# Kernel optimization log

Measured on AMD Instinct MI355X. Metric: run time of the kernel, lower is better.

Reference implementation:

```python
import jax, jax.numpy as jnp
import numpy as np

HEADS = 8
DIM_HEAD = 64
QLEVEL = 127.0  # symmetric int8: clamp to [-128, 127]


def fake_quant(x):
    """Symmetric per-tensor int8 fake quantization with straight-through estimator."""
    delta = jnp.max(jnp.abs(x)) / QLEVEL
    xq = jnp.clip(jnp.round(x / delta), -128.0, 127.0) * delta
    return x + jax.lax.stop_gradient(xq - x)


def setup_inputs() -> dict:
    key = jax.random.key(0)
    ks = jax.random.split(key, 7)
    b, n, m, d, dc = 2, 4096, 1024, 512, 768
    return {
        "x": jax.random.normal(ks[0], (b, n, d), jnp.float32),
        "context": jax.random.normal(ks[1], (b, m, dc), jnp.float32),
        "Wq": jax.random.normal(ks[2], (d, d), jnp.float32) * 0.02,
        "Wk": jax.random.normal(ks[3], (dc, d), jnp.float32) * 0.02,
        "Wv": jax.random.normal(ks[4], (dc, d), jnp.float32) * 0.02,
        "Wo": jax.random.normal(ks[5], (d, d), jnp.float32) * 0.02,
        "bo": jnp.zeros((d,), jnp.float32),
    }


def reference(x, context, Wq, Wk, Wv, Wo, bo):
    b, n, _ = x.shape
    h, dh = HEADS, DIM_HEAD
    scale = dh ** -0.5

    q = x @ Wq            # [b, n, h*dh]
    k = context @ Wk      # [b, m, h*dh]
    v = context @ Wv      # [b, m, h*dh]

    def split(t):  # b n (h d) -> b h n d
        return t.reshape(t.shape[0], t.shape[1], h, dh).transpose(0, 2, 1, 3)

    q, k, v = split(q), split(k), split(v)

    # fake-quantize q and k before the score matmul (use_aq=True path)
    q = fake_quant(q)
    k = fake_quant(k)
    sim = jnp.einsum('bhid,bhjd->bhij', q, k) * scale  # [b, h, n, m]
    attn = jax.nn.softmax(sim, axis=-1)

    # fake-quantize attention weights and v before the AV matmul
    out = jnp.einsum('bhij,bhjd->bhid', fake_quant(attn), fake_quant(v))
    out = out.transpose(0, 2, 1, 3).reshape(b, n, h * dh)  # b h n d -> b n (h d)
    return out @ Wo + bo  # to_out[0]; to_out[-1] is Dropout (identity in eval)
```

## Files before the change

kernel.cpp:

```cpp
#include <hip/hip_runtime.h>
#include <stdint.h>

typedef float  v4f  __attribute__((ext_vector_type(4)));
typedef int    v4i  __attribute__((ext_vector_type(4)));
typedef __bf16 v8bf __attribute__((ext_vector_type(8)));
typedef __bf16 v4bf __attribute__((ext_vector_type(4)));

#define BATCH  2
#define NQ     4096
#define MK     1024
#define DMODEL 512
#define DCTX   768
#define NH     8
#define DH     64

__global__ __launch_bounds__(256) void k_wtrans(
    const float* __restrict__ Wq, const float* __restrict__ Wk,
    const float* __restrict__ Wv, const float* __restrict__ Wo,
    __bf16* __restrict__ Wq_t, __bf16* __restrict__ Wk_t,
    __bf16* __restrict__ Wv_t, __bf16* __restrict__ Wo_t,
    unsigned* __restrict__ scal) {
  if (blockIdx.x == 0 && blockIdx.y == 0 && blockIdx.z == 0 && threadIdx.x < 4)
    scal[threadIdx.x] = 0u;
  const float* src; __bf16* dst; int K;
  switch (blockIdx.z) {
    case 0:  src = Wq; dst = Wq_t; K = DMODEL; break;
    case 1:  src = Wk; dst = Wk_t; K = DCTX;   break;
    case 2:  src = Wv; dst = Wv_t; K = DCTX;   break;
    default: src = Wo; dst = Wo_t; K = DMODEL; break;
  }
  int k0 = blockIdx.y * 32;
  if (k0 >= K) return;
  int n0 = blockIdx.x * 32;
  __shared__ __bf16 tile[32][33];
  int c = threadIdx.x & 31, r0 = threadIdx.x >> 5;
  for (int i = 0; i < 4; ++i) {
    int r = r0 + i * 8;
    tile[c][r] = (__bf16)src[(size_t)(k0 + r) * DMODEL + n0 + c];
  }
  __syncthreads();
  for (int i = 0; i < 4; ++i) {
    int r = r0 + i * 8;
    dst[(size_t)(n0 + r) * K + k0 + c] = tile[r][c];
  }
}

template<bool BIAS, bool AMAX>
__global__ __launch_bounds__(256, 4) void k_gemm64(
    const float* __restrict__ A, const __bf16* __restrict__ Bt,
    float* __restrict__ C, int M, int N, int K,
    const float* __restrict__ bias,
    unsigned* __restrict__ amaxLo, unsigned* __restrict__ amaxHi) {
  __shared__ __bf16 As[64 * 76];
  __shared__ __bf16 Bs[64 * 76];
  __shared__ float redmax[4];
  const int tid = threadIdx.x;
  const int lane = tid & 63, wave = tid >> 6;
  const int l15 = lane & 15, g = lane >> 4;
  const int row0 = blockIdx.x * 64, col0 = blockIdx.y * 64;
  const int wrow = (wave >> 1) * 32, wcol = (wave & 1) * 32;

  v4f acc[2][2] = {};

  for (int k0 = 0; k0 < K; k0 += 64) {
#pragma unroll
    for (int i = 0; i < 4; ++i) {
      int f = tid + 256 * i;
      int r = f >> 4, c4 = (f & 15) << 2;
      float4 av = *(const float4*)(A + (size_t)(row0 + r) * K + k0 + c4);
      v4bf ap = { (__bf16)av.x, (__bf16)av.y, (__bf16)av.z, (__bf16)av.w };
      *(v4bf*)(&As[r * 76 + c4]) = ap;
    }
#pragma unroll
    for (int i = 0; i < 2; ++i) {
      int f = tid + 256 * i;
      int r = f >> 3, c8 = (f & 7) << 3;
      *(v8bf*)(&Bs[r * 76 + c8]) =
          *(const v8bf*)(Bt + (size_t)(col0 + r) * K + k0 + c8);
    }
    __syncthreads();
#pragma unroll
    for (int c = 0; c < 2; ++c) {
      v8bf af0 = *(const v8bf*)(&As[(wrow + l15) * 76 + c * 32 + g * 8]);
      v8bf af1 = *(const v8bf*)(&As[(wrow + 16 + l15) * 76 + c * 32 + g * 8]);
      v8bf bf0 = *(const v8bf*)(&Bs[(wcol + l15) * 76 + c * 32 + g * 8]);
      v8bf bf1 = *(const v8bf*)(&Bs[(wcol + 16 + l15) * 76 + c * 32 + g * 8]);
      acc[0][0] = __builtin_amdgcn_mfma_f32_16x16x32_bf16(af0, bf0, acc[0][0], 0, 0, 0);
      acc[0][1] = __builtin_amdgcn_mfma_f32_16x16x32_bf16(af0, bf1, acc[0][1], 0, 0, 0);
      acc[1][0] = __builtin_amdgcn_mfma_f32_16x16x32_bf16(af1, bf0, acc[1][0], 0, 0, 0);
      acc[1][1] = __builtin_amdgcn_mfma_f32_16x16x32_bf16(af1, bf1, acc[1][1], 0, 0, 0);
    }
    __syncthreads();
  }

  float lmax = 0.0f;
#pragma unroll
  for (int j = 0; j < 2; ++j) {
    int col = col0 + wcol + j * 16 + l15;
    float bv = BIAS ? bias[col] : 0.0f;
#pragma unroll
    for (int i = 0; i < 2; ++i) {
#pragma unroll
      for (int r = 0; r < 4; ++r) {
        int row = row0 + wrow + i * 16 + g * 4 + r;
        float cv = acc[i][j][r] + bv;
        C[(size_t)row * N + col] = cv;
        if (AMAX) lmax = fmaxf(lmax, fabsf(cv));
      }
    }
  }
  if (AMAX) {
    for (int off = 32; off > 0; off >>= 1)
      lmax = fmaxf(lmax, __shfl_xor(lmax, off, 64));
    if (lane == 0) redmax[wave] = lmax;
    __syncthreads();
    if (tid == 0) {
      float bm = fmaxf(fmaxf(redmax[0], redmax[1]), fmaxf(redmax[2], redmax[3]));
      atomicMax(col0 < 512 ? amaxLo : amaxHi, __float_as_uint(bm));
    }
  }
}

__global__ __launch_bounds__(256) void k_quant_all(
    const float* __restrict__ qf, const float* __restrict__ kvf,
    int8_t* __restrict__ q8, int8_t* __restrict__ k8, int8_t* __restrict__ v8t,
    const unsigned* __restrict__ scal) {
  __shared__ int8_t tile[64][80];
  int bx = blockIdx.x;
  if (bx < 5120) {
    float4 v; int8_t* dst; float s;
    if (bx < 4096) {
      int idx = bx * 256 + threadIdx.x;
      v = ((const float4*)qf)[idx];
      dst = q8 + (size_t)idx * 4;
      s = 127.0f / __uint_as_float(scal[0]);
    } else {
      int j = (bx - 4096) * 256 + threadIdx.x;
      int r = j >> 7;
      int c4 = (j & 127) << 2;
      v = *(const float4*)(kvf + (size_t)r * 1024 + c4);
      dst = k8 + (size_t)j * 4;
      s = 127.0f / __uint_as_float(scal[1]);
    }
    int a0 = __float2int_rn(v.x * s), a1 = __float2int_rn(v.y * s);
    int a2 = __float2int_rn(v.z * s), a3 = __float2int_rn(v.w * s);
    a0 = max(-128, min(127, a0)); a1 = max(-128, min(127, a1));
    a2 = max(-128, min(127, a2)); a3 = max(-128, min(127, a3));
    unsigned p = (unsigned)(a0 & 255) | ((unsigned)(a1 & 255) << 8) |
                 ((unsigned)(a2 & 255) << 16) | ((unsigned)(a3 & 255) << 24);
    *(unsigned*)dst = p;
    return;
  }
  int id = bx - 5120;
  int bh = id >> 4, b = bh >> 3, h = bh & 7;
  int j0 = (id & 15) * 64;
  const float s = 127.0f / __uint_as_float(scal[2]);
  int t = threadIdx.x;
  int j = t >> 2, dh0 = (t & 3) << 4;
  const float* src = kvf + (size_t)(b * MK + j0 + j) * 1024 + 512 + h * DH + dh0;
#pragma unroll
  for (int i = 0; i < 16; i += 4) {
    float4 v = *(const float4*)(src + i);
    int a0 = __float2int_rn(v.x * s), a1 = __float2int_rn(v.y * s);
    int a2 = __float2int_rn(v.z * s), a3 = __float2int_rn(v.w * s);
    tile[dh0 + i + 0][j] = (int8_t)max(-128, min(127, a0));
    tile[dh0 + i + 1][j] = (int8_t)max(-128, min(127, a1));
    tile[dh0 + i + 2][j] = (int8_t)max(-128, min(127, a2));
    tile[dh0 + i + 3][j] = (int8_t)max(-128, min(127, a3));
  }
  __syncthreads();
  int dh = t >> 2, jb = (t & 3) << 4;
  v4i val = *(const v4i*)(&tile[dh][jb]);
  *(v4i*)(v8t + (size_t)(bh * DH + dh) * MK + j0 + jb) = val;
}

__global__ __launch_bounds__(256, 4) void k_pass1(
    const int8_t* __restrict__ q8, const int8_t* __restrict__ k8,
    float* __restrict__ invz, unsigned* __restrict__ scal) {
  __shared__ float zbuf[4][64];
  __shared__ int   mbuf[4][64];
  int bh = blockIdx.y, b = bh >> 3, h = bh & 7;
  int wave = threadIdx.x >> 6, lane = threadIdx.x & 63;
  int l15 = lane & 15, g = lane >> 4;
  int row0 = blockIdx.x * 64;
  const float aq = __uint_as_float(scal[0]), ak = __uint_as_float(scal[1]);
  const float alpha2 = (aq * ak) * (0.125f / (127.0f * 127.0f)) * 1.44269504f;
  const v4i z4 = {0, 0, 0, 0};
  v4i qfrag[4];
#pragma unroll
  for (int rg = 0; rg < 4; ++rg)
    qfrag[rg] = *(const v4i*)(q8 + (size_t)(b * NQ + row0 + rg * 16 + l15) * DMODEL + h * DH + g * 16);
  const int8_t* kbase = k8 + (size_t)b * MK * DMODEL + h * DH + g * 16 +
                        (size_t)wave * 256 * DMODEL;
  v4i kf[16];
#pragma unroll
  for (int i = 0; i < 16; ++i)
    kf[i] = *(const v4i*)(kbase + (size_t)(i * 16 + l15) * DMODEL);

  float z[4] = {0.f, 0.f, 0.f, 0.f};
  int mi[4] = {-(1 << 30), -(1 << 30), -(1 << 30), -(1 << 30)};
#pragma unroll
  for (int kt = 0; kt < 16; ++kt) {
#pragma unroll
    for (int rg = 0; rg < 4; ++rg) {
      v4i sa = __builtin_amdgcn_mfma_i32_16x16x64_i8(kf[kt], qfrag[rg], z4, 0, 0, 0);
      mi[rg] = max(mi[rg], max(max(sa[0], sa[1]), max(sa[2], sa[3])));
      float e0 = __builtin_amdgcn_exp2f((float)sa[0] * alpha2);
      float e1 = __builtin_amdgcn_exp2f((float)sa[1] * alpha2);
      float e2 = __builtin_amdgcn_exp2f((float)sa[2] * alpha2);
      float e3 = __builtin_amdgcn_exp2f((float)sa[3] * alpha2);
      z[rg] += (e0 + e1) + (e2 + e3);
    }
  }
#pragma unroll
  for (int rg = 0; rg < 4; ++rg) {
    z[rg] += __shfl_xor(z[rg], 16, 64);
    mi[rg] = max(mi[rg], __shfl_xor(mi[rg], 16, 64));
    z[rg] += __shfl_xor(z[rg], 32, 64);
    mi[rg] = max(mi[rg], __shfl_xor(mi[rg], 32, 64));
  }
  if (lane < 16) {
#pragma unroll
    for (int rg = 0; rg < 4; ++rg) {
      zbuf[wave][rg * 16 + l15] = z[rg];
      mbuf[wave][rg * 16 + l15] = mi[rg];
    }
  }
  __syncthreads();
  if (threadIdx.x < 64) {
    int r = threadIdx.x;
    float zt = (zbuf[0][r] + zbuf[1][r]) + (zbuf[2][r] + zbuf[3][r]);
    int mt = max(max(mbuf[0][r], mbuf[1][r]), max(mbuf[2][r], mbuf[3][r]));
    float iz = 1.0f / zt;
    invz[(size_t)bh * NQ + row0 + r] = iz;
    float ma = __builtin_amdgcn_exp2f((float)mt * alpha2) * iz;
    for (int off = 1; off < 64; off <<= 1)
      ma = fmaxf(ma, __shfl_xor(ma, off, 64));
    if (r == 0) atomicMax(scal + 3, __float_as_uint(ma));
  }
}

__global__ __launch_bounds__(256, 2) void k_pass2(
    const int8_t* __restrict__ q8, const int8_t* __restrict__ k8,
    const int8_t* __restrict__ v8t, const float* __restrict__ invz,
    const unsigned* __restrict__ scal, float* __restrict__ o) {
  __shared__ __align__(16) int8_t attn_lds[4][16 * 80];
  __shared__ __align__(16) int redbuf[16][64][4];
  int bh = blockIdx.y, b = bh >> 3, h = bh & 7;
  int wave = threadIdx.x >> 6, lane = threadIdx.x & 63;
  int l15 = lane & 15, g = lane >> 4;
  int row0 = blockIdx.x * 64;
  int key0 = wave * 256;
  const float aq = __uint_as_float(scal[0]), ak = __uint_as_float(scal[1]);
  const float avv = __uint_as_float(scal[2]), izm = __uint_as_float(scal[3]);
  const float alpha2 = (aq * ak) * (0.125f / (127.0f * 127.0f)) * 1.44269504f;
  const float oscale = (izm / 127.0f) * (avv / 127.0f);
  const float MAGIC = 12582912.0f;
  const v4i z4 = {0, 0, 0, 0};

  v4i qfrag[4];
  float lc[4];
#pragma unroll
  for (int rg = 0; rg < 4; ++rg) {
    qfrag[rg] = *(const v4i*)(q8 + (size_t)(b * NQ + row0 + rg * 16 + l15) * DMODEL + h * DH + g * 16);
    lc[rg] = __builtin_amdgcn_logf(invz[(size_t)bh * NQ + row0 + rg * 16 + l15] * (127.0f / izm));
  }
  const int8_t* kbase = k8 + (size_t)(b * MK + key0) * DMODEL + h * DH + g * 16;
  v4i kf[16];
#pragma unroll
  for (int i = 0; i < 16; ++i)
    kf[i] = *(const v4i*)(kbase + (size_t)(i * 16 + l15) * DMODEL);
  const int8_t* vbase = v8t + (size_t)bh * DH * MK + key0 + g * 16;
  v4i vf[16];
#pragma unroll
  for (int d = 0; d < 4; ++d)
#pragma unroll
    for (int c = 0; c < 4; ++c)
      vf[d * 4 + c] = *(const v4i*)(vbase + (size_t)(d * 16 + l15) * MK + c * 64);

  int8_t* alds = attn_lds[wave];
  float* obase = o + (size_t)(b * NQ + row0) * DMODEL + h * DH;

#pragma unroll
  for (int rg = 0; rg < 4; ++rg) {
    const float lcr = lc[rg];
    v4i pacc[4] = {};
#pragma unroll
    for (int c = 0; c < 4; ++c) {
#pragma unroll
      for (int t = 0; t < 4; ++t) {
        v4i sa = __builtin_amdgcn_mfma_i32_16x16x64_i8(kf[c * 4 + t], qfrag[rg], z4, 0, 0, 0);
        float f0 = __builtin_amdgcn_exp2f(fmaf((float)sa[0], alpha2, lcr)) + MAGIC;
        float f1 = __builtin_amdgcn_exp2f(fmaf((float)sa[1], alpha2, lcr)) + MAGIC;
        float f2 = __builtin_amdgcn_exp2f(fmaf((float)sa[2], alpha2, lcr)) + MAGIC;
        float f3 = __builtin_amdgcn_exp2f(fmaf((float)sa[3], alpha2, lcr)) + MAGIC;
        unsigned packed = (__float_as_uint(f0) & 255u) |
                          ((__float_as_uint(f1) & 255u) << 8) |
                          ((__float_as_uint(f2) & 255u) << 16) |
                          (__float_as_uint(f3) << 24);
        *(unsigned*)(alds + l15 * 80 + t * 16 + g * 4) = packed;
      }
      v4i afrag = *(const v4i*)(alds + l15 * 80 + g * 16);
#pragma unroll
      for (int d = 0; d < 4; ++d)
        pacc[d] = __builtin_amdgcn_mfma_i32_16x16x64_i8(afrag, vf[d * 4 + c], pacc[d], 0, 0, 0);
    }
    __syncthreads();
#pragma unroll
    for (int d = 0; d < 4; ++d)
      *(v4i*)(&redbuf[wave * 4 + d][lane][0]) = pacc[d];
    __syncthreads();
    v4i s0 = *(const v4i*)(&redbuf[wave][lane][0]);
    v4i s1 = *(const v4i*)(&redbuf[4 + wave][lane][0]);
    v4i s2 = *(const v4i*)(&redbuf[8 + wave][lane][0]);
    v4i s3 = *(const v4i*)(&redbuf[12 + wave][lane][0]);
    v4i sum = (s0 + s1) + (s2 + s3);
#pragma unroll
    for (int r = 0; r < 4; ++r) {
      int row = rg * 16 + (lane >> 4) * 4 + r;
      obase[(size_t)row * DMODEL + wave * 16 + (lane & 15)] = (float)sum[r] * oscale;
    }
  }
}

extern "C" void kernel_launch(void* const* d_in, const int* in_sizes, int n_in,
                              void* d_out, int out_size, void* d_ws, size_t ws_size,
                              hipStream_t stream) {
  (void)in_sizes; (void)n_in; (void)out_size; (void)ws_size;
  const float* x   = (const float*)d_in[0];
  const float* ctx = (const float*)d_in[1];
  const float* Wq  = (const float*)d_in[2];
  const float* Wk  = (const float*)d_in[3];
  const float* Wv  = (const float*)d_in[4];
  const float* Wo  = (const float*)d_in[5];
  const float* bo  = (const float*)d_in[6];
  float* out = (float*)d_out;

  char* ws = (char*)d_ws;
  size_t off = 0;
  auto alloc = [&](size_t bytes) {
    char* p = ws + off;
    off += (bytes + 255) & ~(size_t)255;
    return p;
  };
  unsigned* scal = (unsigned*)alloc(16);
  __bf16* Wq_t = (__bf16*)alloc((size_t)512 * 512 * 2);
  __bf16* Wk_t = (__bf16*)alloc((size_t)512 * 768 * 2);
  __bf16* Wv_t = (__bf16*)alloc((size_t)512 * 768 * 2);
  __bf16* Wo_t = (__bf16*)alloc((size_t)512 * 512 * 2);
  float* qf  = (float*)alloc((size_t)BATCH * NQ * DMODEL * 4);
  float* kvf = (float*)alloc((size_t)BATCH * MK * 1024 * 4);
  int8_t* q8 = (int8_t*)alloc((size_t)BATCH * NQ * DMODEL);
  int8_t* k8 = (int8_t*)alloc((size_t)BATCH * MK * DMODEL);
  int8_t* v8t = (int8_t*)alloc((size_t)BATCH * NH * DH * MK);
  float* invz = (float*)alloc((size_t)BATCH * NH * NQ * 4);
  float* o = qf;

  k_wtrans<<<dim3(16, 24, 4), 256, 0, stream>>>(Wq, Wk, Wv, Wo, Wq_t, Wk_t, Wv_t, Wo_t, scal);
  k_gemm64<false, true><<<dim3(128, 8), 256, 0, stream>>>(
      x, Wq_t, qf, 8192, 512, 512, nullptr, scal + 0, scal + 0);
  k_gemm64<false, true><<<dim3(32, 16), 256, 0, stream>>>(
      ctx, Wk_t, kvf, 2048, 1024, 768, nullptr, scal + 1, scal + 2);
  k_quant_all<<<5376, 256, 0, stream>>>(qf, kvf, q8, k8, v8t, scal);
  k_pass1<<<dim3(64, 16), 256, 0, stream>>>(q8, k8, invz, scal);
  k_pass2<<<dim3(64, 16), 256, 0, stream>>>(q8, k8, v8t, invz, scal, o);
  k_gemm64<true, false><<<dim3(128, 8), 256, 0, stream>>>(
      o, Wo_t, out, 8192, 512, 512, bo, nullptr, nullptr);
}
```

Baseline: 210.0 us.

## Fuse Q quantization into pass1, emit bf16 attention output, use 128-row GEMM tiles

Q int8 quantization moves out of the standalone quant kernel and into pass1, which now reads fp32 Q, quantizes its fragments in registers and writes q8 for pass2. That removes one full pass over the Q tensor, leaving the quant kernel to handle only K and V. Pass2 now writes the attention output in bf16, halving that intermediate, and the output GEMM loads bf16 directly with no conversion. The Q and output projections use a templated GEMM with 128-row tiles to improve B-tile reuse, at the cost of more accumulator registers per wave.

```diff
diff --git a/kernel.cpp b/kernel.cpp
--- a/kernel.cpp
+++ b/kernel.cpp
@@ -1,5 +1,6 @@
 #include <hip/hip_runtime.h>
 #include <stdint.h>
+#include <type_traits>
 
 typedef float  v4f  __attribute__((ext_vector_type(4)));
 typedef int    v4i  __attribute__((ext_vector_type(4)));
@@ -45,31 +46,42 @@
   }
 }
 
-template<bool BIAS, bool AMAX>
-__global__ __launch_bounds__(256, 4) void k_gemm64(
-    const float* __restrict__ A, const __bf16* __restrict__ Bt,
+template<int MT, bool BIAS, bool AMAX, typename AT>
+__global__ __launch_bounds__(256, 4) void k_gemm(
+    const AT* __restrict__ A, const __bf16* __restrict__ Bt,
     float* __restrict__ C, int M, int N, int K,
     const float* __restrict__ bias,
     unsigned* __restrict__ amaxLo, unsigned* __restrict__ amaxHi) {
-  __shared__ __bf16 As[64 * 76];
+  constexpr int IT = MT / 32;
+  __shared__ __bf16 As[MT * 76];
   __shared__ __bf16 Bs[64 * 76];
   __shared__ float redmax[4];
   const int tid = threadIdx.x;
   const int lane = tid & 63, wave = tid >> 6;
   const int l15 = lane & 15, g = lane >> 4;
-  const int row0 = blockIdx.x * 64, col0 = blockIdx.y * 64;
-  const int wrow = (wave >> 1) * 32, wcol = (wave & 1) * 32;
-
-  v4f acc[2][2] = {};
+  const int row0 = blockIdx.x * MT, col0 = blockIdx.y * 64;
+  const int wrow = (wave >> 1) * (MT / 2), wcol = (wave & 1) * 32;
+
+  v4f acc[IT][2] = {};
 
   for (int k0 = 0; k0 < K; k0 += 64) {
-#pragma unroll
-    for (int i = 0; i < 4; ++i) {
-      int f = tid + 256 * i;
-      int r = f >> 4, c4 = (f & 15) << 2;
-      float4 av = *(const float4*)(A + (size_t)(row0 + r) * K + k0 + c4);
-      v4bf ap = { (__bf16)av.x, (__bf16)av.y, (__bf16)av.z, (__bf16)av.w };
-      *(v4bf*)(&As[r * 76 + c4]) = ap;
+    if constexpr (std::is_same<AT, float>::value) {
+#pragma unroll
+      for (int i = 0; i < MT / 16; ++i) {
+        int f = tid + 256 * i;
+        int r = f >> 4, c4 = (f & 15) << 2;
+        float4 av = *(const float4*)(A + (size_t)(row0 + r) * K + k0 + c4);
+        v4bf ap = { (__bf16)av.x, (__bf16)av.y, (__bf16)av.z, (__bf16)av.w };
+        *(v4bf*)(&As[r * 76 + c4]) = ap;
+      }
+    } else {
+#pragma unroll
+      for (int i = 0; i < MT / 32; ++i) {
+        int f = tid + 256 * i;
+        int r = f >> 3, c8 = (f & 7) << 3;
+        *(v8bf*)(&As[r * 76 + c8]) =
+            *(const v8bf*)(A + (size_t)(row0 + r) * K + k0 + c8);
+      }
     }
 #pragma unroll
     for (int i = 0; i < 2; ++i) {
@@ -81,14 +93,14 @@
     __syncthreads();
 #pragma unroll
     for (int c = 0; c < 2; ++c) {
-      v8bf af0 = *(const v8bf*)(&As[(wrow + l15) * 76 + c * 32 + g * 8]);
-      v8bf af1 = *(const v8bf*)(&As[(wrow + 16 + l15) * 76 + c * 32 + g * 8]);
       v8bf bf0 = *(const v8bf*)(&Bs[(wcol + l15) * 76 + c * 32 + g * 8]);
       v8bf bf1 = *(const v8bf*)(&Bs[(wcol + 16 + l15) * 76 + c * 32 + g * 8]);
-      acc[0][0] = __builtin_amdgcn_mfma_f32_16x16x32_bf16(af0, bf0, acc[0][0], 0, 0, 0);
-      acc[0][1] = __builtin_amdgcn_mfma_f32_16x16x32_bf16(af0, bf1, acc[0][1], 0, 0, 0);
-      acc[1][0] = __builtin_amdgcn_mfma_f32_16x16x32_bf16(af1, bf0, acc[1][0], 0, 0, 0);
-      acc[1][1] = __builtin_amdgcn_mfma_f32_16x16x32_bf16(af1, bf1, acc[1][1], 0, 0, 0);
+#pragma unroll
+      for (int i = 0; i < IT; ++i) {
+        v8bf af = *(const v8bf*)(&As[(wrow + i * 16 + l15) * 76 + c * 32 + g * 8]);
+        acc[i][0] = __builtin_amdgcn_mfma_f32_16x16x32_bf16(af, bf0, acc[i][0], 0, 0, 0);
+        acc[i][1] = __builtin_amdgcn_mfma_f32_16x16x32_bf16(af, bf1, acc[i][1], 0, 0, 0);
+      }
     }
     __syncthreads();
   }
@@ -99,7 +111,7 @@
     int col = col0 + wcol + j * 16 + l15;
     float bv = BIAS ? bias[col] : 0.0f;
 #pragma unroll
-    for (int i = 0; i < 2; ++i) {
+    for (int i = 0; i < IT; ++i) {
 #pragma unroll
       for (int r = 0; r < 4; ++r) {
         int row = row0 + wrow + i * 16 + g * 4 + r;
@@ -121,37 +133,28 @@
   }
 }
 
-__global__ __launch_bounds__(256) void k_quant_all(
-    const float* __restrict__ qf, const float* __restrict__ kvf,
-    int8_t* __restrict__ q8, int8_t* __restrict__ k8, int8_t* __restrict__ v8t,
+__global__ __launch_bounds__(256) void k_quant_kv(
+    const float* __restrict__ kvf,
+    int8_t* __restrict__ k8, int8_t* __restrict__ v8t,
     const unsigned* __restrict__ scal) {
   __shared__ int8_t tile[64][80];
   int bx = blockIdx.x;
-  if (bx < 5120) {
-    float4 v; int8_t* dst; float s;
-    if (bx < 4096) {
-      int idx = bx * 256 + threadIdx.x;
-      v = ((const float4*)qf)[idx];
-      dst = q8 + (size_t)idx * 4;
-      s = 127.0f / __uint_as_float(scal[0]);
-    } else {
-      int j = (bx - 4096) * 256 + threadIdx.x;
-      int r = j >> 7;
-      int c4 = (j & 127) << 2;
-      v = *(const float4*)(kvf + (size_t)r * 1024 + c4);
-      dst = k8 + (size_t)j * 4;
-      s = 127.0f / __uint_as_float(scal[1]);
-    }
+  if (bx < 1024) {
+    int j = bx * 256 + threadIdx.x;
+    int r = j >> 7;
+    int c4 = (j & 127) << 2;
+    float4 v = *(const float4*)(kvf + (size_t)r * 1024 + c4);
+    float s = 127.0f / __uint_as_float(scal[1]);
     int a0 = __float2int_rn(v.x * s), a1 = __float2int_rn(v.y * s);
     int a2 = __float2int_rn(v.z * s), a3 = __float2int_rn(v.w * s);
     a0 = max(-128, min(127, a0)); a1 = max(-128, min(127, a1));
     a2 = max(-128, min(127, a2)); a3 = max(-128, min(127, a3));
     unsigned p = (unsigned)(a0 & 255) | ((unsigned)(a1 & 255) << 8) |
                  ((unsigned)(a2 & 255) << 16) | ((unsigned)(a3 & 255) << 24);
-    *(unsigned*)dst = p;
+    *(unsigned*)(k8 + (size_t)j * 4) = p;
     return;
   }
-  int id = bx - 5120;
+  int id = bx - 1024;
   int bh = id >> 4, b = bh >> 3, h = bh & 7;
   int j0 = (id & 15) * 64;
   const float s = 127.0f / __uint_as_float(scal[2]);
@@ -174,8 +177,24 @@
   *(v4i*)(v8t + (size_t)(bh * DH + dh) * MK + j0 + jb) = val;
 }
 
+__device__ __forceinline__ v4i quant_pack16(const float* p, float s) {
+  v4i out;
+#pragma unroll
+  for (int q = 0; q < 4; ++q) {
+    float4 v = *(const float4*)(p + q * 4);
+    int a0 = __float2int_rn(v.x * s), a1 = __float2int_rn(v.y * s);
+    int a2 = __float2int_rn(v.z * s), a3 = __float2int_rn(v.w * s);
+    a0 = max(-128, min(127, a0)); a1 = max(-128, min(127, a1));
+    a2 = max(-128, min(127, a2)); a3 = max(-128, min(127, a3));
+    out[q] = (int)((unsigned)(a0 & 255) | ((unsigned)(a1 & 255) << 8) |
+                   ((unsigned)(a2 & 255) << 16) | ((unsigned)(a3 & 255) << 24));
+  }
+  return out;
+}
+
 __global__ __launch_bounds__(256, 4) void k_pass1(
-    const int8_t* __restrict__ q8, const int8_t* __restrict__ k8,
+    const float* __restrict__ qf, int8_t* __restrict__ q8,
+    const int8_t* __restrict__ k8,
     float* __restrict__ invz, unsigned* __restrict__ scal) {
   __shared__ float zbuf[4][64];
   __shared__ int   mbuf[4][64];
@@ -185,11 +204,15 @@
   int row0 = blockIdx.x * 64;
   const float aq = __uint_as_float(scal[0]), ak = __uint_as_float(scal[1]);
   const float alpha2 = (aq * ak) * (0.125f / (127.0f * 127.0f)) * 1.44269504f;
+  const float sq = 127.0f / aq;
   const v4i z4 = {0, 0, 0, 0};
   v4i qfrag[4];
 #pragma unroll
-  for (int rg = 0; rg < 4; ++rg)
-    qfrag[rg] = *(const v4i*)(q8 + (size_t)(b * NQ + row0 + rg * 16 + l15) * DMODEL + h * DH + g * 16);
+  for (int rg = 0; rg < 4; ++rg) {
+    size_t off = (size_t)(b * NQ + row0 + rg * 16 + l15) * DMODEL + h * DH + g * 16;
+    qfrag[rg] = quant_pack16(qf + off, sq);
+    *(v4i*)(q8 + off) = qfrag[rg];
+  }
   const int8_t* kbase = k8 + (size_t)b * MK * DMODEL + h * DH + g * 16 +
                         (size_t)wave * 256 * DMODEL;
   v4i kf[16];
@@ -243,7 +266,7 @@
 __global__ __launch_bounds__(256, 2) void k_pass2(
     const int8_t* __restrict__ q8, const int8_t* __restrict__ k8,
     const int8_t* __restrict__ v8t, const float* __restrict__ invz,
-    const unsigned* __restrict__ scal, float* __restrict__ o) {
+    const unsigned* __restrict__ scal, __bf16* __restrict__ o) {
   __shared__ __align__(16) int8_t attn_lds[4][16 * 80];
   __shared__ __align__(16) int redbuf[16][64][4];
   int bh = blockIdx.y, b = bh >> 3, h = bh & 7;
@@ -279,7 +302,7 @@
       vf[d * 4 + c] = *(const v4i*)(vbase + (size_t)(d * 16 + l15) * MK + c * 64);
 
   int8_t* alds = attn_lds[wave];
-  float* obase = o + (size_t)(b * NQ + row0) * DMODEL + h * DH;
+  __bf16* obase = o + (size_t)(b * NQ + row0) * DMODEL + h * DH;
 
 #pragma unroll
   for (int rg = 0; rg < 4; ++rg) {
@@ -318,7 +341,8 @@
 #pragma unroll
     for (int r = 0; r < 4; ++r) {
       int row = rg * 16 + (lane >> 4) * 4 + r;
-      obase[(size_t)row * DMODEL + wave * 16 + (lane & 15)] = (float)sum[r] * oscale;
+      obase[(size_t)row * DMODEL + wave * 16 + (lane & 15)] =
+          (__bf16)((float)sum[r] * oscale);
     }
   }
 }
@@ -354,16 +378,16 @@
   int8_t* k8 = (int8_t*)alloc((size_t)BATCH * MK * DMODEL);
   int8_t* v8t = (int8_t*)alloc((size_t)BATCH * NH * DH * MK);
   float* invz = (float*)alloc((size_t)BATCH * NH * NQ * 4);
-  float* o = qf;
+  __bf16* o = (__bf16*)qf;
 
   k_wtrans<<<dim3(16, 24, 4), 256, 0, stream>>>(Wq, Wk, Wv, Wo, Wq_t, Wk_t, Wv_t, Wo_t, scal);
-  k_gemm64<false, true><<<dim3(128, 8), 256, 0, stream>>>(
+  k_gemm<128, false, true, float><<<dim3(64, 8), 256, 0, stream>>>(
       x, Wq_t, qf, 8192, 512, 512, nullptr, scal + 0, scal + 0);
-  k_gemm64<false, true><<<dim3(32, 16), 256, 0, stream>>>(
+  k_gemm<64, false, true, float><<<dim3(32, 16), 256, 0, stream>>>(
       ctx, Wk_t, kvf, 2048, 1024, 768, nullptr, scal + 1, scal + 2);
-  k_quant_all<<<5376, 256, 0, stream>>>(qf, kvf, q8, k8, v8t, scal);
-  k_pass1<<<dim3(64, 16), 256, 0, stream>>>(q8, k8, invz, scal);
+  k_quant_kv<<<1280, 256, 0, stream>>>(kvf, k8, v8t, scal);
+  k_pass1<<<dim3(64, 16), 256, 0, stream>>>(qf, q8, k8, invz, scal);
   k_pass2<<<dim3(64, 16), 256, 0, stream>>>(q8, k8, v8t, invz, scal, o);
-  k_gemm64<true, false><<<dim3(128, 8), 256, 0, stream>>>(
+  k_gemm<128, true, false, __bf16><<<dim3(64, 8), 256, 0, stream>>>(
       o, Wo_t, out, 8192, 512, 512, bo, nullptr, nullptr);
 }
```

Measured after the change: 219.9 us. +4.7%, slower.
